# Performance work log

Hardware: AMD Instinct MI355X
Metric: run time of the kernel (lower is better)

Reference implementation:

```python
import jax, jax.numpy as jnp
import numpy as np

# NSA hyperparams (match init_kwargs)
KS, ST, SEL, TOPN, WIN = 32, 16, 64, 16, 512
NEG = -1e30  # additive mask value (finite so fp32 softmax stays stable)


def setup_inputs() -> dict:
    key = jax.random.key(0)
    ks = jax.random.split(key, 6)
    B, S, Hq, Hk, D, Dv = 1, 2048, 16, 2, 128, 128
    q = jax.random.normal(ks[0], (B, S, Hq, D), jnp.float32)
    k = jax.random.normal(ks[1], (B, S, Hk, D), jnp.float32)
    v = jax.random.normal(ks[2], (B, S, Hk, Dv), jnp.float32)
    # learned per-position compression weights for K and V blocks
    w_cmp_k = jax.random.normal(ks[3], (KS,), jnp.float32) / KS
    w_cmp_v = jax.random.normal(ks[4], (KS,), jnp.float32) / KS
    # gating head: Linear(qk_head_dim, 3) -> sigmoid
    w_gate = jax.random.normal(ks[5], (D, 3), jnp.float32) * 0.02
    b_gate = jnp.zeros((3,), jnp.float32)
    return dict(q=q, k=k, v=v, w_cmp_k=w_cmp_k, w_cmp_v=w_cmp_v,
                w_gate=w_gate, b_gate=b_gate)


def _nsa(q, k, v, w_cmp_k, w_cmp_v, w_gate, b_gate):
    B, S, Hq, D = q.shape
    Hk = k.shape[2]
    G = Hq // Hk                      # GQA group size
    Dv = v.shape[-1]
    scale = D ** -0.5
    t_pos = jnp.arange(S)

    # ---- 1. compressed-KV attention (CompressAttn) ----
    T = (S - KS) // ST + 1            # number of compressed blocks
    widx = jnp.arange(T)[:, None] * ST + jnp.arange(KS)[None, :]   # [T, KS]
    cmp_k = jnp.einsum('btknd,k->btnd', k[:, widx], w_cmp_k)        # [B,T,Hk,D]
    cmp_v = jnp.einsum('btknd,k->btnd', v[:, widx], w_cmp_v)        # [B,T,Hk,Dv]

    qg = q.reshape(B, S, Hk, G, D)
    s_cmp = jnp.einsum('bsngd,btnd->bngst', qg, cmp_k) * scale      # [B,Hk,G,S,T]
    blk_end = jnp.arange(T) * ST + KS - 1
    cmp_mask = blk_end[None, :] <= t_pos[:, None]                   # [S,T] block fully past
    p_cmp = jax.nn.softmax(jnp.where(cmp_mask, s_cmp, NEG), axis=-1)
    p_cmp = p_cmp * cmp_mask          # zero rows with no visible block
    cmp_o = jnp.einsum('bngst,btnd->bsngd', p_cmp, cmp_v).reshape(B, S, Hq, Dv)

    # ---- 2. top-n selection-block scoring (select_for_fwd_bwd) ----
    NSel = S // SEL
    starts = jnp.arange(T) * ST
    b_lo = starts // SEL
    b_hi = (starts + KS - 1) // SEL
    bidx = jnp.arange(NSel)
    # map compressed-block probs onto overlapping selection blocks
    Mmap = ((bidx[None, :] >= b_lo[:, None]) & (bidx[None, :] <= b_hi[:, None])).astype(q.dtype)  # [T,NSel]
    p_slc = jnp.einsum('bngst,tm->bnsm', p_cmp, Mmap)               # sum over group g -> [B,Hk,S,NSel]

    cur_blk = t_pos // SEL
    blk_causal = (bidx[None, :] * SEL) <= t_pos[:, None]            # [S,NSel]
    forced = (bidx[None, :] == 0) | (bidx[None, :] == cur_blk[:, None])
    blk_score = jnp.where(forced, -NEG, p_slc)                      # always keep block 0 + current
    blk_score = jnp.where(blk_causal, blk_score, NEG)
    vals, inds = jax.lax.top_k(blk_score, TOPN)                     # [B,Hk,S,TOPN]
    valid = (vals > NEG / 2).astype(q.dtype)
    sel_blk_mask = (jax.nn.one_hot(inds, NSel, dtype=q.dtype) * valid[..., None]).sum(-2) > 0  # [B,Hk,S,NSel]

    # ---- 3. block-sparse selected attention (select_attn) ----
    tok_sel_mask = jnp.repeat(sel_blk_mask, SEL, axis=-1)           # [B,Hk,S,S]
    causal = t_pos[None, :] <= t_pos[:, None]                       # [S,S]
    tok_sel_mask = tok_sel_mask & causal
    s_tok = jnp.einsum('bsngd,bjnd->bngsj', qg, k) * scale          # [B,Hk,G,S,S] shared scores
    p_sel = jax.nn.softmax(jnp.where(tok_sel_mask[:, :, None], s_tok, NEG), axis=-1)
    sel_o = jnp.einsum('bngsj,bjnd->bsngd', p_sel, v).reshape(B, S, Hq, Dv)

    win_mask = causal & ((t_pos[:, None] - t_pos[None, :]) <= WIN)
    p_win = jax.nn.softmax(jnp.where(win_mask, s_tok, NEG), axis=-1)
    win_o = jnp.einsum('bngsj,bjnd->bsngd', p_win, v).reshape(B, S, Hq, Dv)

    # ---- 5. learned sigmoid gating combine ----
    gate = jax.nn.sigmoid(jnp.einsum('bshd,dc->bshc', q, w_gate) + b_gate)  # [B,S,Hq,3]
    return (cmp_o * gate[..., 0:1] + sel_o * gate[..., 1:2] + win_o * gate[..., 2:3])


def reference(q, k, v, w_cmp_k, w_cmp_v, w_gate, b_gate):
    return _nsa(q, k, v, w_cmp_k, w_cmp_v, w_gate, b_gate)
```

## Files before the change

### kernel.cpp

```cpp
#include <hip/hip_runtime.h>

#define SS   2048
#define HQ   16
#define HK   2
#define GQ   8
#define DD   128
#define DV   128
#define KS   32
#define ST   16
#define SELB 64
#define TOPN 16
#define WINW 512
#define TT   127
#define NSEL 32
#define SCALE 0.08838834764831845f

typedef __attribute__((ext_vector_type(8))) short bf16x8;
typedef __attribute__((ext_vector_type(4))) short short4v;
typedef __attribute__((ext_vector_type(4))) float f32x4;

__device__ __forceinline__ short f2bf(float x) {
    union { float f; unsigned u; } a; a.f = x;
    unsigned r = a.u + 0x7FFFu + ((a.u >> 16) & 1u);
    return (short)(r >> 16);
}
__device__ __forceinline__ float bf2f(short b) {
    union { unsigned u; float f; } x; x.u = ((unsigned)(unsigned short)b) << 16; return x.f;
}

__global__ __launch_bounds__(256) void k_prep(
    const float* __restrict__ k, const float* __restrict__ v,
    const float* __restrict__ wck, const float* __restrict__ wcv,
    short* __restrict__ kfr, short* __restrict__ vfr,
    short* __restrict__ ckh, short* __restrict__ ckl,
    short* __restrict__ cvfr)
{
    int bid = blockIdx.x, tid = threadIdx.x;
    int lane = tid & 63, quad = (lane >> 4) & 3, l16 = lane & 15;
    if (bid < 256) {
        int tb = bid >> 1, n = bid & 1;
        int kb = tid >> 6;
        int token = tb * 16 + l16;
        int feat = kb * 32 + quad * 8;
        const float* src = &k[(token * HK + n) * DD + feat];
        bf16x8 t;
        #pragma unroll
        for (int e = 0; e < 8; ++e) t[e] = f2bf(src[e]);
        *(bf16x8*)&kfr[(((n * 128 + tb) * 4 + kb) * 64 + lane) * 8] = t;
    } else if (bid < 320) {
        int id = bid - 256;
        int cb = id >> 1, n = id & 1;
        #pragma unroll
        for (int it = 0; it < 4; ++it) {
            int frag = it * 4 + (tid >> 6);
            int h = frag >> 3, f = frag & 7;
            int d = f * 16 + l16;
            int tok0 = cb * 64 + h * 32 + quad * 8;
            bf16x8 t;
            #pragma unroll
            for (int e = 0; e < 8; ++e) t[e] = f2bf(v[((tok0 + e) * HK + n) * DV + d]);
            *(bf16x8*)&vfr[((((n * 32 + cb) * 2 + h) * 8 + f) * 64 + lane) * 8] = t;
        }
    } else if (bid < 576) {
        int id = bid - 320;
        int n = id & 1, t = id >> 1;
        if (tid < 128) {
            int d = tid;
            float a = 0.f;
            if (t < TT) {
                for (int j = 0; j < KS; ++j)
                    a += k[((t * ST + j) * HK + n) * DD + d] * wck[j];
            }
            short hi = f2bf(a);
            short lo = f2bf(a - bf2f(hi));
            int tile = t >> 4, l16i = t & 15;
            int kb = d >> 5, qd = (d >> 3) & 3, e = d & 7;
            int off = (((n * 8 + tile) * 4 + kb) * 64 + qd * 16 + l16i) * 8 + e;
            ckh[off] = hi;
            ckl[off] = lo;
        }
    } else {
        int id = bid - 576;
        int n = id & 1, tok = id >> 1;
        if (tid < 128) {
            int d = tid;
            float a = 0.f;
            if (tok < TT) {
                for (int j = 0; j < KS; ++j)
                    a += v[((tok * ST + j) * HK + n) * DV + d] * wcv[j];
            }
            int w2 = d >> 5, half = (d >> 4) & 1, l16i = d & 15;
            int kb = tok >> 5, qd = (tok >> 3) & 3, e = tok & 7;
            cvfr[((((n * 4 + w2) * 2 + half) * 4 + kb) * 64 + qd * 16 + l16i) * 8 + e] = f2bf(a);
        }
    }
}

__global__ __launch_bounds__(256, 4) void k_fused(
    const float* __restrict__ q,
    const short* __restrict__ ckh, const short* __restrict__ ckl,
    const short* __restrict__ cvfr,
    const short* __restrict__ kfr, const short* __restrict__ vfr,
    const float* __restrict__ wg, const float* __restrict__ bg,
    float* __restrict__ out)
{
    int s0 = (SS - 2) - (int)blockIdx.x * 2;
    int s1 = s0 + 1;
    int n = blockIdx.y;
    int tid = threadIdx.x;
    int w = tid >> 6, lane = tid & 63, quad = lane >> 4, l16 = lane & 15;

    __shared__ union {
        struct {
            float qs[16][132];
            float p[16][128];
            short Pt[16][136];
        } c;
        union {
            short Pw[4][16][72];
            float o_lds[2][16][132];
        } f;
    } u;
    __shared__ short cmpO[16][136];
    __shared__ short OselB[16][128];
    __shared__ float g3v[16][3];
    __shared__ float pslc2[2][NSEL];
    __shared__ float lw[4][16];
    __shared__ unsigned selMask[2];
    __shared__ unsigned ublk[NSEL];
    __shared__ int shUCnt;

    f32x4 z4 = {0.f, 0.f, 0.f, 0.f};

    for (int i = tid; i < 16 * 128; i += 256) {
        int row = i >> 7, d = i & 127;
        u.c.qs[row][d] = q[((s0 + (row >> 3)) * HQ + n * GQ + (row & 7)) * DD + d];
    }
    __syncthreads();

    bf16x8 qb[4];
    bf16x8 qlb[4];
    {
        const float* qp = &u.c.qs[l16][quad * 8];
        #pragma unroll
        for (int kb = 0; kb < 4; ++kb) {
            f32x4 x = *(const f32x4*)(qp + kb * 32);
            f32x4 y = *(const f32x4*)(qp + kb * 32 + 4);
            bf16x8 th, tl;
            #pragma unroll
            for (int j = 0; j < 4; ++j) {
                th[j] = f2bf(x[j]);     tl[j] = f2bf(x[j] - bf2f(th[j]));
                th[4+j] = f2bf(y[j]);   tl[4+j] = f2bf(y[j] - bf2f(th[4+j]));
            }
            qb[kb] = th; qlb[kb] = tl;
        }
    }
    if (tid < 48) {
        int h2 = tid / 3, c = tid % 3;
        float a = 0.f;
        for (int d2 = 0; d2 < DD; ++d2) a += u.c.qs[h2][d2] * wg[d2 * 3 + c];
        a += bg[c];
        g3v[h2][c] = 1.f / (1.f + __expf(-a));
    }
    for (int tile = w; tile < 8; tile += 4) {
        const short* khp = &ckh[((n * 8 + tile) * 256 + lane) * 8];
        const short* klp = &ckl[((n * 8 + tile) * 256 + lane) * 8];
        f32x4 acc = z4;
        #pragma unroll
        for (int kb = 0; kb < 4; ++kb) {
            bf16x8 ah = *(const bf16x8*)(khp + kb * 512);
            bf16x8 al = *(const bf16x8*)(klp + kb * 512);
            acc = __builtin_amdgcn_mfma_f32_16x16x32_bf16(ah, qb[kb], acc, 0, 0, 0);
            acc = __builtin_amdgcn_mfma_f32_16x16x32_bf16(al, qb[kb], acc, 0, 0, 0);
            acc = __builtin_amdgcn_mfma_f32_16x16x32_bf16(ah, qlb[kb], acc, 0, 0, 0);
        }
        f32x4 sv;
        #pragma unroll
        for (int r = 0; r < 4; ++r) sv[r] = acc[r] * SCALE;
        *(f32x4*)&u.c.p[l16][tile * 16 + quad * 4] = sv;
    }
    __syncthreads();

    int ntt0 = (s0 >= KS - 1) ? min((s0 - (KS - 1)) / ST + 1, TT) : 0;
    int ntt1 = (s1 >= KS - 1) ? min((s1 - (KS - 1)) / ST + 1, TT) : 0;

    #pragma unroll
    for (int rr = 0; rr < 4; ++rr) {
        int row = w * 4 + rr;
        int ntt = (row < 8) ? ntt0 : ntt1;
        int t1 = lane, t2 = lane + 64;
        float v1 = (t1 < ntt) ? u.c.p[row][t1] : -1e30f;
        float v2 = (t2 < ntt) ? u.c.p[row][t2] : -1e30f;
        float m = fmaxf(v1, v2);
        #pragma unroll
        for (int o = 32; o > 0; o >>= 1) m = fmaxf(m, __shfl_xor(m, o, 64));
        float e1 = (t1 < ntt) ? __expf(v1 - m) : 0.f;
        float e2 = (t2 < ntt) ? __expf(v2 - m) : 0.f;
        float ssum = e1 + e2;
        #pragma unroll
        for (int o = 32; o > 0; o >>= 1) ssum += __shfl_xor(ssum, o, 64);
        float inv = (ntt > 0) ? (1.f / ssum) : 0.f;
        e1 *= inv; e2 *= inv;
        u.c.p[row][t1] = e1; u.c.p[row][t2] = e2;
        u.c.Pt[row][t1] = f2bf(e1); u.c.Pt[row][t2] = f2bf(e2);
    }
    __syncthreads();

    if (tid < 64) {
        int p01 = tid >> 5, m = tid & 31;
        float a = 0.f;
        for (int dt = -1; dt < 4; ++dt) {
            int t = 4 * m + dt;
            if (t < 0 || t >= TT) continue;
            bool maps = (t / 4 == m) || ((t % 4 == 3) && (t / 4 == m - 1));
            if (!maps) continue;
            for (int g = 0; g < GQ; ++g) a += u.c.p[p01 * 8 + g][t];
        }
        pslc2[p01][m] = a;
    }
    __syncthreads();

    if (w < 2) {
        int p01 = w;
        int sp = p01 ? s1 : s0;
        int cur = sp / SELB;
        float v;
        if (lane < NSEL) {
            int m = lane;
            if (m == 0 || m == cur) v = 1e30f;
            else if (m * SELB <= sp) v = pslc2[p01][m];
            else v = -1e30f;
        } else v = -1e31f;
        unsigned msk = 0;
        #pragma unroll
        for (int pick = 0; pick < TOPN; ++pick) {
            float bv = v;
            #pragma unroll
            for (int o = 32; o > 0; o >>= 1) bv = fmaxf(bv, __shfl_xor(bv, o, 64));
            unsigned long long b = __ballot(v == bv);
            int best = __ffsll((long long)b) - 1;
            if (bv > -5e29f) msk |= 1u << best;
            if (lane == best) v = -1e31f;
        }
        if (lane == 0) selMask[p01] = msk;
    }
    {
        f32x4 o0 = z4, o1 = z4;
        int d0 = w * 32 + l16;
        const short* cvp = &cvfr[((n * 4 + w) * 512 + lane) * 8];
        #pragma unroll
        for (int kb = 0; kb < 4; ++kb) {
            bf16x8 pa = *(const bf16x8*)&u.c.Pt[l16][kb * 32 + quad * 8];
            bf16x8 vb0 = *(const bf16x8*)(cvp + kb * 512);
            bf16x8 vb1 = *(const bf16x8*)(cvp + 2048 + kb * 512);
            o0 = __builtin_amdgcn_mfma_f32_16x16x32_bf16(pa, vb0, o0, 0, 0, 0);
            o1 = __builtin_amdgcn_mfma_f32_16x16x32_bf16(pa, vb1, o1, 0, 0, 0);
        }
        #pragma unroll
        for (int r = 0; r < 4; ++r) {
            int h2 = quad * 4 + r;
            cmpO[h2][d0]      = f2bf(o0[r]);
            cmpO[h2][d0 + 16] = f2bf(o1[r]);
        }
    }
    __syncthreads();

    if (tid == 0) {
        unsigned m0 = selMask[0], m1 = selMask[1], mu = m0 | m1;
        int uc = 0;
        for (int b = 0; b < NSEL; ++b)
            if ((mu >> b) & 1u)
                ublk[uc++] = (unsigned)(b * SELB) | (((m0 >> b) & 1u) << 30) | (((m1 >> b) & 1u) << 31);
        shUCnt = uc;
    }
    __syncthreads();
    int uCnt = shUCnt;
    int j00 = (s0 >= WINW) ? (s0 - WINW) : 0;
    int j01 = (s1 >= WINW) ? (s1 - WINW) : 0;
    int tb0 = j00 & ~63;
    int nBlkB = ((s1 - tb0) >> 6) + 1;

    int sLim = (l16 < 8) ? s0 : s1;
    f32x4 o[8];
    float lold;

    auto run_chunks = [&](int nB, bool selMode) {
        #pragma unroll
        for (int f = 0; f < 8; ++f) o[f] = z4;
        lold = 0.f;
        int loWin = selMode ? 0 : ((l16 < 8) ? j00 : j01);
        for (int bi = w; bi < nB; bi += 4) {
            int tstart, vis;
            if (selMode) {
                unsigned e = ublk[bi];
                tstart = (int)(e & 0x0FFFFFFFu);
                vis = (l16 < 8) ? (int)((e >> 30) & 1u) : (int)(e >> 31);
            } else {
                tstart = tb0 + bi * 64;
                vis = 1;
            }
            f32x4 a4[4] = {z4, z4, z4, z4};
            {
                const short* kp = &kfr[((n * 128 + (tstart >> 4)) * 256 + lane) * 8];
                bf16x8 kf[2][4];
                #pragma unroll
                for (int t2 = 0; t2 < 2; ++t2)
                    #pragma unroll
                    for (int kb = 0; kb < 4; ++kb)
                        kf[t2][kb] = *(const bf16x8*)(kp + (t2 * 4 + kb) * 512);
                #pragma unroll
                for (int kb = 0; kb < 4; ++kb) {
                    a4[0] = __builtin_amdgcn_mfma_f32_16x16x32_bf16(kf[0][kb], qb[kb], a4[0], 0, 0, 0);
                    a4[1] = __builtin_amdgcn_mfma_f32_16x16x32_bf16(kf[1][kb], qb[kb], a4[1], 0, 0, 0);
                }
                #pragma unroll
                for (int t2 = 0; t2 < 2; ++t2)
                    #pragma unroll
                    for (int kb = 0; kb < 4; ++kb)
                        kf[t2][kb] = *(const bf16x8*)(kp + ((2 + t2) * 4 + kb) * 512);
                #pragma unroll
                for (int kb = 0; kb < 4; ++kb) {
                    a4[2] = __builtin_amdgcn_mfma_f32_16x16x32_bf16(kf[0][kb], qb[kb], a4[2], 0, 0, 0);
                    a4[3] = __builtin_amdgcn_mfma_f32_16x16x32_bf16(kf[1][kb], qb[kb], a4[3], 0, 0, 0);
                }
            }
            const short* vp = &vfr[((n * 32 + (tstart >> 6)) * 1024 + lane) * 8];
            bf16x8 vf[8];
            #pragma unroll
            for (int f = 0; f < 8; ++f) vf[f] = *(const bf16x8*)(vp + f * 512);
            {
                int lo = loWin - tstart;
                int hi = vis ? (sLim - tstart) : (lo - 1);
                int rngS = hi - lo + 1;
                unsigned rng = (unsigned)(rngS > 0 ? rngS : 0);
                int tb = quad * 4 - lo;
                #pragma unroll
                for (int tile = 0; tile < 4; ++tile) {
                    float ev[4];
                    #pragma unroll
                    for (int r = 0; r < 4; ++r) {
                        unsigned uu = (unsigned)(tb + tile * 16 + r);
                        float ex = __expf(a4[tile][r] * SCALE);
                        ev[r] = (uu < rng) ? ex : 0.f;
                    }
                    lold += (ev[0] + ev[1]) + (ev[2] + ev[3]);
                    unsigned plo = (__float_as_uint(ev[1]) & 0xFFFF0000u) | (__float_as_uint(ev[0]) >> 16);
                    unsigned phi = (__float_as_uint(ev[3]) & 0xFFFF0000u) | (__float_as_uint(ev[2]) >> 16);
                    uint2 pk; pk.x = plo; pk.y = phi;
                    *(uint2*)&u.f.Pw[w][l16][tile * 16 + quad * 4] = pk;
                }
            }
            __builtin_amdgcn_s_waitcnt(0xC07F);
            bf16x8 pa0 = *(const bf16x8*)&u.f.Pw[w][l16][quad * 8];
            bf16x8 pa1 = *(const bf16x8*)&u.f.Pw[w][l16][32 + quad * 8];
            #pragma unroll
            for (int f = 0; f < 8; ++f)
                o[f] = __builtin_amdgcn_mfma_f32_16x16x32_bf16(pa0, vf[f], o[f], 0, 0, 0);
            #pragma unroll
            for (int f = 0; f < 8; ++f)
                o[f] = __builtin_amdgcn_mfma_f32_16x16x32_bf16(pa1, *(const bf16x8*)(vp + (8 + f) * 512), o[f], 0, 0, 0);
        }
    };

    auto combine = [&](bool isA) {
        float lsum = lold;
        lsum += __shfl_xor(lsum, 16, 64);
        lsum += __shfl_xor(lsum, 32, 64);
        if (quad == 0) lw[w][l16] = lsum;
        __syncthreads();
        if (w >= 2) {
            #pragma unroll
            for (int f = 0; f < 8; ++f)
                #pragma unroll
                for (int r = 0; r < 4; ++r)
                    u.f.o_lds[w - 2][quad * 4 + r][l16 + 16 * f] = o[f][r];
        }
        __syncthreads();
        float ltot = lw[0][l16] + lw[1][l16] + lw[2][l16] + lw[3][l16];
        float linv = 1.f / ltot;
        float linvr[4];
        #pragma unroll
        for (int r = 0; r < 4; ++r) linvr[r] = __shfl(linv, quad * 4 + r, 64);
        if (w < 2) {
            #pragma unroll
            for (int f = 0; f < 8; ++f)
                #pragma unroll
                for (int r = 0; r < 4; ++r)
                    o[f][r] += u.f.o_lds[w][quad * 4 + r][l16 + 16 * f];
        }
        __syncthreads();
        if (w == 1) {
            #pragma unroll
            for (int f = 0; f < 8; ++f)
                #pragma unroll
                for (int r = 0; r < 4; ++r)
                    u.f.o_lds[0][quad * 4 + r][l16 + 16 * f] = o[f][r];
        }
        __syncthreads();
        if (w == 0) {
            #pragma unroll
            for (int f = 0; f < 8; ++f)
                #pragma unroll
                for (int r = 0; r < 4; ++r)
                    o[f][r] += u.f.o_lds[0][quad * 4 + r][l16 + 16 * f];
            if (isA) {
                #pragma unroll
                for (int f = 0; f < 8; ++f)
                    #pragma unroll
                    for (int r = 0; r < 4; ++r)
                        OselB[quad * 4 + r][l16 + 16 * f] = f2bf(o[f][r] * linvr[r]);
            } else {
                #pragma unroll
                for (int f = 0; f < 8; ++f)
                    #pragma unroll
                    for (int r = 0; r < 4; ++r) {
                        int h2 = quad * 4 + r;
                        int p = h2 >> 3, g = h2 & 7;
                        int d = l16 + 16 * f;
                        int ob = ((s0 + p) * HQ + n * GQ + g) * DV + d;
                        float owin = o[f][r] * linvr[r];
                        out[ob] = g3v[h2][0] * bf2f(cmpO[h2][d]) + g3v[h2][1] * bf2f(OselB[h2][d]) + g3v[h2][2] * owin;
                    }
            }
        }
        __syncthreads();
    };

    run_chunks(uCnt, true);
    combine(true);
    run_chunks(nBlkB, false);
    combine(false);
}

extern "C" void kernel_launch(void* const* d_in, const int* in_sizes, int n_in,
                              void* d_out, int out_size, void* d_ws, size_t ws_size,
                              hipStream_t stream) {
    const float* q   = (const float*)d_in[0];
    const float* k   = (const float*)d_in[1];
    const float* v   = (const float*)d_in[2];
    const float* wck = (const float*)d_in[3];
    const float* wcv = (const float*)d_in[4];
    const float* wg  = (const float*)d_in[5];
    const float* bg  = (const float*)d_in[6];
    float* out = (float*)d_out;

    short* kfr  = (short*)d_ws;
    short* vfr  = kfr + 2 * 128 * 4 * 64 * 8;
    short* ckh  = vfr + 2 * 32 * 2 * 8 * 64 * 8;
    short* ckl  = ckh + 2 * 8 * 4 * 64 * 8;
    short* cvfr = ckl + 2 * 8 * 4 * 64 * 8;

    k_prep<<<832, 256, 0, stream>>>(k, v, wck, wcv, kfr, vfr, ckh, ckl, cvfr);
    k_fused<<<dim3(SS / 2, HK), 256, 0, stream>>>(q, ckh, ckl, cvfr, kfr, vfr, wg, bg, out);
}
```

Before: 171.6 us.

## Accumulate gated branch outputs directly into global output and rebalance prep blocks

```diff
diff --git a/kernel.cpp b/kernel.cpp
--- a/kernel.cpp
+++ b/kernel.cpp
@@ -47,52 +47,47 @@
         #pragma unroll
         for (int e = 0; e < 8; ++e) t[e] = f2bf(src[e]);
         *(bf16x8*)&kfr[(((n * 128 + tb) * 4 + kb) * 64 + lane) * 8] = t;
-    } else if (bid < 320) {
+    } else if (bid < 512) {
         int id = bid - 256;
-        int cb = id >> 1, n = id & 1;
-        #pragma unroll
-        for (int it = 0; it < 4; ++it) {
-            int frag = it * 4 + (tid >> 6);
-            int h = frag >> 3, f = frag & 7;
-            int d = f * 16 + l16;
-            int tok0 = cb * 64 + h * 32 + quad * 8;
-            bf16x8 t;
-            #pragma unroll
-            for (int e = 0; e < 8; ++e) t[e] = f2bf(v[((tok0 + e) * HK + n) * DV + d]);
-            *(bf16x8*)&vfr[((((n * 32 + cb) * 2 + h) * 8 + f) * 64 + lane) * 8] = t;
-        }
-    } else if (bid < 576) {
-        int id = bid - 320;
-        int n = id & 1, t = id >> 1;
-        if (tid < 128) {
-            int d = tid;
-            float a = 0.f;
-            if (t < TT) {
-                for (int j = 0; j < KS; ++j)
-                    a += k[((t * ST + j) * HK + n) * DD + d] * wck[j];
-            }
-            short hi = f2bf(a);
-            short lo = f2bf(a - bf2f(hi));
-            int tile = t >> 4, l16i = t & 15;
-            int kb = d >> 5, qd = (d >> 3) & 3, e = d & 7;
-            int off = (((n * 8 + tile) * 4 + kb) * 64 + qd * 16 + l16i) * 8 + e;
-            ckh[off] = hi;
-            ckl[off] = lo;
-        }
+        int n = id & 1, cb = (id >> 1) & 31, it = id >> 6;
+        int frag = it * 4 + (tid >> 6);
+        int h = frag >> 3, f = frag & 7;
+        int d = f * 16 + l16;
+        int tok0 = cb * 64 + h * 32 + quad * 8;
+        bf16x8 t;
+        #pragma unroll
+        for (int e = 0; e < 8; ++e) t[e] = f2bf(v[((tok0 + e) * HK + n) * DV + d]);
+        *(bf16x8*)&vfr[((((n * 32 + cb) * 2 + h) * 8 + f) * 64 + lane) * 8] = t;
+    } else if (bid < 640) {
+        int id = bid - 512;
+        int n = id & 1;
+        int t = (id >> 1) * 2 + (tid >> 7);
+        int d = tid & 127;
+        float a = 0.f;
+        if (t < TT) {
+            for (int j = 0; j < KS; ++j)
+                a += k[((t * ST + j) * HK + n) * DD + d] * wck[j];
+        }
+        short hi = f2bf(a);
+        short lo = f2bf(a - bf2f(hi));
+        int tile = t >> 4, l16i = t & 15;
+        int kb = d >> 5, qd = (d >> 3) & 3, e = d & 7;
+        int off = (((n * 8 + tile) * 4 + kb) * 64 + qd * 16 + l16i) * 8 + e;
+        ckh[off] = hi;
+        ckl[off] = lo;
     } else {
-        int id = bid - 576;
-        int n = id & 1, tok = id >> 1;
-        if (tid < 128) {
-            int d = tid;
-            float a = 0.f;
-            if (tok < TT) {
-                for (int j = 0; j < KS; ++j)
-                    a += v[((tok * ST + j) * HK + n) * DV + d] * wcv[j];
-            }
-            int w2 = d >> 5, half = (d >> 4) & 1, l16i = d & 15;
-            int kb = tok >> 5, qd = (tok >> 3) & 3, e = tok & 7;
-            cvfr[((((n * 4 + w2) * 2 + half) * 4 + kb) * 64 + qd * 16 + l16i) * 8 + e] = f2bf(a);
-        }
+        int id = bid - 640;
+        int n = id & 1;
+        int tok = (id >> 1) * 2 + (tid >> 7);
+        int d = tid & 127;
+        float a = 0.f;
+        if (tok < TT) {
+            for (int j = 0; j < KS; ++j)
+                a += v[((tok * ST + j) * HK + n) * DV + d] * wcv[j];
+        }
+        int w2 = d >> 5, half = (d >> 4) & 1, l16i = d & 15;
+        int kb = tok >> 5, qd = (tok >> 3) & 3, e = tok & 7;
+        cvfr[((((n * 4 + w2) * 2 + half) * 4 + kb) * 64 + qd * 16 + l16i) * 8 + e] = f2bf(a);
     }
 }
 
@@ -121,8 +116,6 @@
             float o_lds[2][16][132];
         } f;
     } u;
-    __shared__ short cmpO[16][136];
-    __shared__ short OselB[16][128];
     __shared__ float g3v[16][3];
     __shared__ float pslc2[2][NSEL];
     __shared__ float lw[4][16];
@@ -259,8 +252,11 @@
         #pragma unroll
         for (int r = 0; r < 4; ++r) {
             int h2 = quad * 4 + r;
-            cmpO[h2][d0]      = f2bf(o0[r]);
-            cmpO[h2][d0 + 16] = f2bf(o1[r]);
+            int p = h2 >> 3, g = h2 & 7;
+            int ob = ((s0 + p) * HQ + n * GQ + g) * DV + d0;
+            float g0 = g3v[h2][0];
+            out[ob]      = g0 * o0[r];
+            out[ob + 16] = g0 * o1[r];
         }
     }
     __syncthreads();
@@ -398,30 +394,18 @@
         }
         __syncthreads();
         if (w == 0) {
-            #pragma unroll
-            for (int f = 0; f < 8; ++f)
-                #pragma unroll
-                for (int r = 0; r < 4; ++r)
-                    o[f][r] += u.f.o_lds[0][quad * 4 + r][l16 + 16 * f];
-            if (isA) {
-                #pragma unroll
-                for (int f = 0; f < 8; ++f)
-                    #pragma unroll
-                    for (int r = 0; r < 4; ++r)
-                        OselB[quad * 4 + r][l16 + 16 * f] = f2bf(o[f][r] * linvr[r]);
-            } else {
-                #pragma unroll
-                for (int f = 0; f < 8; ++f)
-                    #pragma unroll
-                    for (int r = 0; r < 4; ++r) {
-                        int h2 = quad * 4 + r;
-                        int p = h2 >> 3, g = h2 & 7;
-                        int d = l16 + 16 * f;
-                        int ob = ((s0 + p) * HQ + n * GQ + g) * DV + d;
-                        float owin = o[f][r] * linvr[r];
-                        out[ob] = g3v[h2][0] * bf2f(cmpO[h2][d]) + g3v[h2][1] * bf2f(OselB[h2][d]) + g3v[h2][2] * owin;
-                    }
-            }
+            int gi = isA ? 1 : 2;
+            #pragma unroll
+            for (int f = 0; f < 8; ++f)
+                #pragma unroll
+                for (int r = 0; r < 4; ++r) {
+                    int h2 = quad * 4 + r;
+                    int p = h2 >> 3, g = h2 & 7;
+                    int d = l16 + 16 * f;
+                    int ob = ((s0 + p) * HQ + n * GQ + g) * DV + d;
+                    float val = (o[f][r] + u.f.o_lds[0][h2][l16 + 16 * f]) * linvr[r];
+                    out[ob] += g3v[h2][gi] * val;
+                }
         }
         __syncthreads();
     };
@@ -450,6 +434,6 @@
     short* ckl  = ckh + 2 * 8 * 4 * 64 * 8;
     short* cvfr = ckl + 2 * 8 * 4 * 64 * 8;
 
-    k_prep<<<832, 256, 0, stream>>>(k, v, wck, wcv, kfr, vfr, ckh, ckl, cvfr);
+    k_prep<<<768, 256, 0, stream>>>(k, v, wck, wcv, kfr, vfr, ckh, ckl, cvfr);
     k_fused<<<dim3(SS / 2, HK), 256, 0, stream>>>(q, ckh, ckl, cvfr, kfr, vfr, wg, bg, out);
 }
```

Measured after the change: 186.9 us. 8.9% more time.
